# Kernel optimization log

Measured on AMD Instinct MI355X. Metric: run time of the kernel, lower is better.

## Reference

```python
import jax, jax.numpy as jnp
import numpy as np

# NVFP4 e2m1 representable magnitudes and nearest-rounding decision boundaries
FP4_GRID = jnp.array([0.0, 0.5, 1.0, 1.5, 2.0, 3.0, 4.0, 6.0], dtype=jnp.float32)
FP4_BOUNDS = jnp.array([0.25, 0.75, 1.25, 1.75, 2.5, 3.5, 5.0], dtype=jnp.float32)
E4M3_MAX = 448.0
FP4_MAX = 6.0
BLOCK = 16  # NVFP4 block size along K


def round_fp4(x):
    """Round to nearest FP4 (e2m1) representable value (saturating at +-6)."""
    idx = jnp.searchsorted(FP4_BOUNDS, jnp.abs(x))
    return jnp.sign(x) * FP4_GRID[idx]


def cast_e4m3(x):
    """Saturating cast through float8_e4m3fn and back to fp32."""
    return jnp.clip(x, -E4M3_MAX, E4M3_MAX).astype(jnp.float8_e4m3fn).astype(jnp.float32)


def setup_inputs() -> dict:
    key = jax.random.key(0)
    kx, kw, kb = jax.random.split(key, 3)
    M, N, K = 32, 8192, 8192
    x = jax.random.normal(kx, (M, K), dtype=jnp.float32)
    w = jax.random.normal(kw, (N, K), dtype=jnp.float32)
    bias = jax.random.normal(kb, (N,), dtype=jnp.float32)

    # raw global scales: amax / (448 * 6)  (== 1 / fp4_global_scale)
    weight_scale_2 = jnp.max(jnp.abs(w)) / (E4M3_MAX * FP4_MAX)
    input_scale = jnp.max(jnp.abs(x)) / (E4M3_MAX * FP4_MAX)

    # offline NVFP4 quantization of the weight (as done in __init__)
    wb = w.reshape(N, K // BLOCK, BLOCK)
    sf = jnp.max(jnp.abs(wb), axis=-1) / FP4_MAX              # [N, K//16] per-block scale
    weight_scale = cast_e4m3(sf / weight_scale_2)             # fp8 block scales (values)
    dscale = weight_scale[..., None] * weight_scale_2         # per-element dequant scale
    safe = jnp.where(dscale > 0, dscale, 1.0)
    w_fp4 = jnp.where(dscale > 0, round_fp4(wb / safe), 0.0).reshape(N, K)

    return {
        "x": x,
        "weight_fp4": w_fp4,
        "bias": bias,
        "input_scale": input_scale.reshape(1),
        "weight_scale": weight_scale,
        "weight_scale_2": weight_scale_2.reshape(1),
    }


def reference(x, weight_fp4, bias, input_scale, weight_scale, weight_scale_2):
    N, K = weight_fp4.shape
    M = x.shape[0]
    # --- weight dequant: fp4 value * fp8 block scale * global scale ---
    w_dq = (weight_fp4.reshape(N, K // BLOCK, BLOCK)
            * weight_scale[..., None] * weight_scale_2).reshape(N, K)
    # --- dynamic NVFP4 fake-quant of the activation ---
    xb = x.reshape(M, K // BLOCK, BLOCK)
    sf = cast_e4m3(jnp.max(jnp.abs(xb), axis=-1) / FP4_MAX / input_scale)  # [M, K//16]
    scale = sf[..., None] * input_scale                                    # per-element scale
    safe = jnp.where(scale > 0, scale, 1.0)
    x_dq = jnp.where(scale > 0, round_fp4(xb / safe) * scale, 0.0).reshape(M, K)
    # --- linear ---
    return x_dq @ w_dq.T + bias
```

## Files before the change

kernel.cpp:

```cpp
#include <hip/hip_runtime.h>

typedef float f32x4 __attribute__((ext_vector_type(4)));
typedef short s16x8 __attribute__((ext_vector_type(8)));

#define M_DIM 32
#define N_DIM 8192
#define K_DIM 8192
#define NBLK (K_DIM / 16)
#define KSPLIT 4
#define WSTEPS 16
#define SCL_LD 129

__device__ inline unsigned short f2bf(float f) {
    unsigned int u = __float_as_uint(f);
    u = (u + 0x7FFFu + ((u >> 16) & 1u)) >> 16;
    return (unsigned short)u;
}

__device__ inline float round_fp4(float x) {
    float a = fabsf(x);
    float g;
    if (a > 2.5f)        g = (a > 5.0f) ? 6.0f : ((a > 3.5f) ? 4.0f : 3.0f);
    else if (a > 1.25f)  g = (a > 1.75f) ? 2.0f : 1.5f;
    else                 g = (a > 0.75f) ? 1.0f : ((a > 0.25f) ? 0.5f : 0.0f);
    return copysignf(g, x);
}

__device__ inline float cast_e4m3(float v) {
    v = fminf(v, 448.0f);
    if (v < 0.015625f) {
        return rintf(v * 512.0f) * (1.0f / 512.0f);
    }
    int e; float m = frexpf(v, &e);
    return ldexpf(rintf(m * 16.0f) * 0.0625f, e);
}

__global__ void init_out(const float* __restrict__ bias, float* __restrict__ out) {
    int i = blockIdx.x * blockDim.x + threadIdx.x;
    f32x4 b = *(const f32x4*)(bias + ((i * 4) & (N_DIM - 1)));
    *(f32x4*)(out + (size_t)i * 4) = b;
}

__global__ void quant_pack_x(const float* __restrict__ x,
                             const float* __restrict__ input_scale,
                             unsigned short* __restrict__ xpack) {
    int tid = blockIdx.x * blockDim.x + threadIdx.x;
    int m = tid >> 9;
    int b = tid & 511;
    const float is = input_scale[0];

    const float* xp = x + (size_t)m * K_DIM + b * 16;
    f32x4 l0 = *(const f32x4*)(xp);
    f32x4 l1 = *(const f32x4*)(xp + 4);
    f32x4 l2 = *(const f32x4*)(xp + 8);
    f32x4 l3 = *(const f32x4*)(xp + 12);
    float v[16];
    #pragma unroll
    for (int i = 0; i < 4; ++i) { v[i]=l0[i]; v[4+i]=l1[i]; v[8+i]=l2[i]; v[12+i]=l3[i]; }

    float amax = 0.f;
    #pragma unroll
    for (int i = 0; i < 16; ++i) amax = fmaxf(amax, fabsf(v[i]));

    float sf = cast_e4m3(amax / 6.0f / is);
    float scale = sf * is;

    int kstep = b >> 1;
    int t = m >> 4;
    int mrow = m & 15;
    unsigned short* base = xpack + (size_t)kstep * 1024 + t * 512;
    #pragma unroll
    for (int i = 0; i < 16; ++i) {
        float q = 0.f;
        if (scale > 0.f) q = round_fp4(v[i] / scale) * scale;
        int g = ((b & 1) << 1) + (i >> 3);
        int lane = g * 16 + mrow;
        int j = i & 7;
        base[lane * 8 + j] = f2bf(q);
    }
}

__global__ __launch_bounds__(256, 8) void gemm_kernel(
    const float* __restrict__ W,
    const float* __restrict__ wscale,
    const float* __restrict__ ws2p,
    const unsigned short* __restrict__ xpack,
    float* __restrict__ out)
{
    __shared__ float shm[16 * SCL_LD];

    const int wave = threadIdx.x >> 6;
    const int lane = threadIdx.x & 63;
    const int lrow = lane & 15;
    const int lgrp = lane >> 4;
    const int n0 = blockIdx.x * 16;
    const int kb = blockIdx.y;
    const float ws2 = ws2p[0];

    {
        int t = threadIdx.x;
        int row = t >> 4;
        int c0 = (t & 15) * 8;
        const float* s = wscale + (size_t)(n0 + row) * NBLK + kb * 128 + c0;
        #pragma unroll
        for (int j = 0; j < 8; ++j)
            shm[row * SCL_LD + c0 + j] = s[j] * ws2;
    }
    __syncthreads();

    const int kofs = kb * 2048 + wave * 512;
    const float* wcur = W + (size_t)(n0 + lrow) * K_DIM + kofs + lgrp * 8;
    const unsigned short* xcur = xpack + (size_t)(kofs >> 5) * 1024 + lane * 8;
    const float* sbase = shm + lrow * SCL_LD + wave * 32 + (lgrp >> 1);

    f32x4 acc0 = {0,0,0,0}, acc1 = {0,0,0,0};

    f32x4 a0 = *(const f32x4*)(wcur);
    f32x4 a1 = *(const f32x4*)(wcur + 4);
    s16x8 b0 = *(const s16x8*)(xcur);
    s16x8 b1 = *(const s16x8*)(xcur + 512);

    #pragma unroll
    for (int s = 0; s < WSTEPS; ++s) {
        f32x4 na0, na1; s16x8 nb0, nb1;
        if (s + 1 < WSTEPS) {
            na0 = *(const f32x4*)(wcur + 32);
            na1 = *(const f32x4*)(wcur + 36);
            nb0 = *(const s16x8*)(xcur + 1024);
            nb1 = *(const s16x8*)(xcur + 1536);
        }
        float sc = sbase[s * 2];
        s16x8 af;
        #pragma unroll
        for (int j = 0; j < 4; ++j) {
            af[j]     = (short)f2bf(a0[j] * sc);
            af[4 + j] = (short)f2bf(a1[j] * sc);
        }
        acc0 = __builtin_amdgcn_mfma_f32_16x16x32_bf16(af, b0, acc0, 0, 0, 0);
        acc1 = __builtin_amdgcn_mfma_f32_16x16x32_bf16(af, b1, acc1, 0, 0, 0);
        a0 = na0; a1 = na1; b0 = nb0; b1 = nb1;
        wcur += 32;
        xcur += 1024;
    }

    __syncthreads();
    float* red = shm;
    #pragma unroll
    for (int r = 0; r < 4; ++r) {
        red[wave * 512 + lane * 8 + r]     = acc0[r];
        red[wave * 512 + lane * 8 + 4 + r] = acc1[r];
    }
    __syncthreads();

    #pragma unroll
    for (int h = 0; h < 2; ++h) {
        int j = threadIdx.x + h * 256;
        float v = red[j] + red[512 + j] + red[1024 + j] + red[1536 + j];
        int l = j >> 3, t = (j >> 2) & 1, r = j & 3;
        int m = t * 16 + (l & 15);
        int n = n0 + ((l >> 4) << 2) + r;
        atomicAdd(out + (size_t)m * N_DIM + n, v);
    }
}

extern "C" void kernel_launch(void* const* d_in, const int* in_sizes, int n_in,
                              void* d_out, int out_size, void* d_ws, size_t ws_size,
                              hipStream_t stream) {
    const float* x           = (const float*)d_in[0];
    const float* weight_fp4  = (const float*)d_in[1];
    const float* bias        = (const float*)d_in[2];
    const float* input_scale = (const float*)d_in[3];
    const float* wscale      = (const float*)d_in[4];
    const float* ws2         = (const float*)d_in[5];
    float* out = (float*)d_out;
    unsigned short* xpack = (unsigned short*)d_ws;

    init_out<<<256, 256, 0, stream>>>(bias, out);
    quant_pack_x<<<64, 256, 0, stream>>>(x, input_scale, xpack);
    gemm_kernel<<<dim3(512, KSPLIT), 256, 0, stream>>>(weight_fp4, wscale, ws2, xpack, out);
}
```

Measured before the change: 73.72 us.

## Stage weight tiles through LDS with async global_load_lds double buffering

The GEMM kernel now copies weight rows into a double-buffered LDS tile with asynchronous global-to-LDS loads, instead of loading them directly into registers. It uses 8 waves per block with a K-split of 2 rather than 4 waves with a K-split of 4, which halves the atomic adds to the output. Block scales are read straight from global memory each step instead of being preloaded into shared memory. The intent is to get coalesced, overlapped weight streaming. In exchange it adds a __syncthreads per tile, needs 33KB of LDS per block (which limits occupancy), and the cross-wave reduction is now 8-way.

```diff
diff --git a/kernel.cpp b/kernel.cpp
--- a/kernel.cpp
+++ b/kernel.cpp
@@ -7,9 +7,12 @@
 #define N_DIM 8192
 #define K_DIM 8192
 #define NBLK (K_DIM / 16)
-#define KSPLIT 4
-#define WSTEPS 16
-#define SCL_LD 129
+#define KSPLIT 2
+#define BLK_K 4096
+#define TILE_K 256
+#define NTILES (BLK_K / TILE_K)
+#define ROW_STRIDE 1040
+#define SLOT_BYTES (16 * ROW_STRIDE)
 
 __device__ inline unsigned short f2bf(float f) {
     unsigned int u = __float_as_uint(f);
@@ -33,6 +36,11 @@
     }
     int e; float m = frexpf(v, &e);
     return ldexpf(rintf(m * 16.0f) * 0.0625f, e);
+}
+
+__device__ __forceinline__ void async_copy16(const void* g, void* l) {
+    __builtin_amdgcn_global_load_lds((const __attribute__((address_space(1))) void*)g,
+                                     (__attribute__((address_space(3))) void*)l, 16, 0, 0);
 }
 
 __global__ void init_out(const float* __restrict__ bias, float* __restrict__ out) {
@@ -80,14 +88,14 @@
     }
 }
 
-__global__ __launch_bounds__(256, 8) void gemm_kernel(
+__global__ __launch_bounds__(512, 8) void gemm_kernel(
     const float* __restrict__ W,
     const float* __restrict__ wscale,
     const float* __restrict__ ws2p,
     const unsigned short* __restrict__ xpack,
     float* __restrict__ out)
 {
-    __shared__ float shm[16 * SCL_LD];
+    __shared__ __align__(16) unsigned char lds[2 * SLOT_BYTES];
 
     const int wave = threadIdx.x >> 6;
     const int lane = threadIdx.x & 63;
@@ -97,39 +105,34 @@
     const int kb = blockIdx.y;
     const float ws2 = ws2p[0];
 
-    {
-        int t = threadIdx.x;
-        int row = t >> 4;
-        int c0 = (t & 15) * 8;
-        const float* s = wscale + (size_t)(n0 + row) * NBLK + kb * 128 + c0;
-        #pragma unroll
-        for (int j = 0; j < 8; ++j)
-            shm[row * SCL_LD + c0 + j] = s[j] * ws2;
-    }
-    __syncthreads();
+    const float* wsrc0 = W + (size_t)(n0 + 2 * wave)     * K_DIM + kb * BLK_K + lane * 4;
+    const float* wsrc1 = W + (size_t)(n0 + 2 * wave + 1) * K_DIM + kb * BLK_K + lane * 4;
 
-    const int kofs = kb * 2048 + wave * 512;
-    const float* wcur = W + (size_t)(n0 + lrow) * K_DIM + kofs + lgrp * 8;
-    const unsigned short* xcur = xpack + (size_t)(kofs >> 5) * 1024 + lane * 8;
-    const float* sbase = shm + lrow * SCL_LD + wave * 32 + (lgrp >> 1);
+    auto stage = [&](int t) {
+        unsigned char* slot = lds + (t & 1) * SLOT_BYTES;
+        async_copy16(wsrc0 + t * TILE_K, slot + (2 * wave)     * ROW_STRIDE);
+        async_copy16(wsrc1 + t * TILE_K, slot + (2 * wave + 1) * ROW_STRIDE);
+    };
+
+    const int S0 = kb * 128 + wave;
+    const unsigned short* xcur = xpack + (size_t)S0 * 1024 + lane * 8;
+    const float* scur = wscale + (size_t)(n0 + lrow) * NBLK + S0 * 2 + (lgrp >> 1);
+    const int aoff = wave * 128 + lgrp * 32;
 
     f32x4 acc0 = {0,0,0,0}, acc1 = {0,0,0,0};
 
-    f32x4 a0 = *(const f32x4*)(wcur);
-    f32x4 a1 = *(const f32x4*)(wcur + 4);
-    s16x8 b0 = *(const s16x8*)(xcur);
-    s16x8 b1 = *(const s16x8*)(xcur + 512);
+    stage(0);
+    __syncthreads();
 
-    #pragma unroll
-    for (int s = 0; s < WSTEPS; ++s) {
-        f32x4 na0, na1; s16x8 nb0, nb1;
-        if (s + 1 < WSTEPS) {
-            na0 = *(const f32x4*)(wcur + 32);
-            na1 = *(const f32x4*)(wcur + 36);
-            nb0 = *(const s16x8*)(xcur + 1024);
-            nb1 = *(const s16x8*)(xcur + 1536);
-        }
-        float sc = sbase[s * 2];
+    #pragma unroll 2
+    for (int t = 0; t < NTILES; ++t) {
+        if (t + 1 < NTILES) stage(t + 1);
+        const unsigned char* slot = lds + (t & 1) * SLOT_BYTES;
+        f32x4 a0 = *(const f32x4*)(slot + lrow * ROW_STRIDE + aoff);
+        f32x4 a1 = *(const f32x4*)(slot + lrow * ROW_STRIDE + aoff + 16);
+        s16x8 b0 = *(const s16x8*)(xcur);
+        s16x8 b1 = *(const s16x8*)(xcur + 512);
+        float sc = *scur * ws2;
         s16x8 af;
         #pragma unroll
         for (int j = 0; j < 4; ++j) {
@@ -138,13 +141,12 @@
         }
         acc0 = __builtin_amdgcn_mfma_f32_16x16x32_bf16(af, b0, acc0, 0, 0, 0);
         acc1 = __builtin_amdgcn_mfma_f32_16x16x32_bf16(af, b1, acc1, 0, 0, 0);
-        a0 = na0; a1 = na1; b0 = nb0; b1 = nb1;
-        wcur += 32;
-        xcur += 1024;
+        xcur += 8 * 1024;
+        scur += 16;
+        __syncthreads();
     }
 
-    __syncthreads();
-    float* red = shm;
+    float* red = (float*)lds;
     #pragma unroll
     for (int r = 0; r < 4; ++r) {
         red[wave * 512 + lane * 8 + r]     = acc0[r];
@@ -152,10 +154,11 @@
     }
     __syncthreads();
 
-    #pragma unroll
-    for (int h = 0; h < 2; ++h) {
-        int j = threadIdx.x + h * 256;
-        float v = red[j] + red[512 + j] + red[1024 + j] + red[1536 + j];
+    {
+        int j = threadIdx.x;
+        float v = 0.f;
+        #pragma unroll
+        for (int w = 0; w < 8; ++w) v += red[w * 512 + j];
         int l = j >> 3, t = (j >> 2) & 1, r = j & 3;
         int m = t * 16 + (l & 15);
         int n = n0 + ((l >> 4) << 2) + r;
@@ -177,5 +180,5 @@
 
     init_out<<<256, 256, 0, stream>>>(bias, out);
     quant_pack_x<<<64, 256, 0, stream>>>(x, input_scale, xpack);
-    gemm_kernel<<<dim3(512, KSPLIT), 256, 0, stream>>>(weight_fp4, wscale, ws2, xpack, out);
+    gemm_kernel<<<dim3(512, KSPLIT), 512, 0, stream>>>(weight_fp4, wscale, ws2, xpack, out);
 }
```

Result: no change. 75.13 us (+1.9%).
